# Kernel optimization log

Measured on AMD Instinct MI355X. Metric: run time of the kernel, lower is better.

## Reference

```python
import jax, jax.numpy as jnp
import numpy as np

L_OUTPUT = 1024  # SequenceDecoder l_output


def setup_inputs() -> dict:
    key = jax.random.key(0)
    k1, k2, k3 = jax.random.split(key, 3)
    B, L, D, DO = 16, 4096, 1024, 1024
    x = jax.random.normal(k1, (B, L, D), dtype=jnp.float32)
    # 0/1 padding-style mask; valid_length = mask.sum(axis=1)
    attention_mask = jax.random.randint(k2, (B, L), 0, 2, dtype=jnp.int32)
    # nn.Linear(d_model, d_output): weight (DO, D), bias (DO,)
    W = jax.random.normal(k3, (DO, D), dtype=jnp.float32) * (1.0 / np.sqrt(D))
    b = jnp.zeros((DO,), dtype=jnp.float32)
    return {"x": x, "attention_mask": attention_mask, "W": W, "b": b}


def _restrict_last(x, attention_mask, l_output):
    """Vectorized equivalent of the per-sample Python loop in mode='last':
    for each batch row i, take the LAST s_i = min(valid_len_i, l_output)
    elements of the full sequence, zero-padded at the tail to l_output.
    (When all s_i == l_output this matches x[:, -l_output:, :], which is the
    only case the original torch.stack-based loop handles without error.)"""
    B, L, D = x.shape
    valid = attention_mask.sum(axis=1)                    # (B,)
    s = jnp.minimum(valid, l_output)                      # (B,)
    j = jnp.arange(l_output)                              # (l_output,)
    idx = jnp.clip(L - s[:, None] + j[None, :], 0, L - 1) # (B, l_output)
    gathered = jnp.take_along_axis(x, idx[:, :, None], axis=1)  # (B, l_output, D)
    keep = (j[None, :] < s[:, None])[:, :, None]          # (B, l_output, 1)
    return jnp.where(keep, gathered, jnp.zeros((), dtype=x.dtype))


def reference(x, attention_mask, W, b):
    # mode='last' restrict, then output_transform = nn.Linear(d_model, d_output)
    restricted = _restrict_last(x, attention_mask, L_OUTPUT)  # (B, l_output, D)
    return jnp.einsum('bld,od->blo', restricted, W) + b       # (B, l_output, DO)
```

## Files before the change

### kernel.cpp

```cpp
#include <hip/hip_runtime.h>
#include <hip/hip_bf16.h>

#define L_SEQ   4096
#define D_IN    1024
#define N_BATCH 16
#define L_OUT   1024
#define D_OUT   1024
#define M_DIM   (N_BATCH * L_OUT)
#define K_DIM   D_IN

#define BM 256
#define BN 256
#define BK 64
#define NKT (K_DIM / BK)

typedef __attribute__((ext_vector_type(4))) float  f32x4;
typedef __attribute__((ext_vector_type(8))) __bf16 bf16x8;
typedef __attribute__((ext_vector_type(4))) __bf16 bf16x4;

#define WS_A_OFF 0u
#define WS_W_OFF (32u * 1024u * 1024u)
#define WS_S_OFF (WS_W_OFF + 2u * 1024u * 1024u)

__global__ __launch_bounds__(256) void mask_sum_kernel(
    const int* __restrict__ mask, int* __restrict__ s_out)
{
    const int b = blockIdx.x;
    const int t = threadIdx.x;
    const int* row = mask + (size_t)b * L_SEQ;

    int sum = 0;
#pragma unroll
    for (int i = 0; i < L_SEQ / 256; ++i) sum += row[t + i * 256];

#pragma unroll
    for (int off = 32; off > 0; off >>= 1) sum += __shfl_down(sum, off, 64);

    __shared__ int wsum[4];
    if ((t & 63) == 0) wsum[t >> 6] = sum;
    __syncthreads();
    if (t == 0) {
        int total = wsum[0] + wsum[1] + wsum[2] + wsum[3];
        s_out[b] = total < L_OUT ? total : L_OUT;
    }
}

__global__ __launch_bounds__(256) void convert_kernel(
    const float* __restrict__ x,
    const float* __restrict__ W,
    const int*   __restrict__ s_arr,
    __bf16* __restrict__ wsA,
    __bf16* __restrict__ wsW)
{
    const int rid = blockIdx.x;
    const int t   = threadIdx.x;
    const int e0  = t * 4;

    if (rid < M_DIM) {
        const int b = rid >> 10;
        const int j = rid & (L_OUT - 1);
        const int s = s_arr[b];
        const int rsw  = (rid & 7) << 3;
        const int dste = (e0 & ~63) | ((e0 & 63) ^ rsw);
        __bf16* dst = wsA + (size_t)rid * K_DIM + dste;
        if (j < s) {
            const float* src = x + ((size_t)b * L_SEQ + (L_SEQ - s + j)) * D_IN + e0;
            f32x4 v = *(const f32x4*)src;
            bf16x4 o = {(__bf16)v.x, (__bf16)v.y, (__bf16)v.z, (__bf16)v.w};
            *(bf16x4*)dst = o;
        } else {
            bf16x4 o = {(__bf16)0.f, (__bf16)0.f, (__bf16)0.f, (__bf16)0.f};
            *(bf16x4*)dst = o;
        }
    } else {
        const int n = rid - M_DIM;
        const int rsw  = (n & 7) << 3;
        const int dste = (e0 & ~63) | ((e0 & 63) ^ rsw);
        const float* src = W + (size_t)n * D_IN + e0;
        f32x4 v = *(const f32x4*)src;
        bf16x4 o = {(__bf16)v.x, (__bf16)v.y, (__bf16)v.z, (__bf16)v.w};
        *(bf16x4*)(wsW + (size_t)n * K_DIM + dste) = o;
    }
}

__device__ __forceinline__ void gload16(const __bf16* g, __bf16* l) {
    __builtin_amdgcn_global_load_lds(
        (const __attribute__((address_space(1))) void*)g,
        (__attribute__((address_space(3))) void*)l,
        16, 0, 0);
}

#define FENCE() asm volatile("" ::: "memory")

__global__ __launch_bounds__(512, 2) void gemm_kernel(
    const __bf16* __restrict__ A,
    const __bf16* __restrict__ Wb,
    const float*  __restrict__ bias,
    float* __restrict__ out)
{
    __shared__ __bf16 smem[2][2][BM * BK];

    const int t  = threadIdx.x;
    const int bx = blockIdx.x;
    const int vb = (bx & 7) * 32 + (bx >> 3);
    const int tile_n = vb & 3;
    const int tile_m = vb >> 2;
    const int m0 = tile_m * BM;
    const int n0 = tile_n * BN;
    const int lane = t & 63;
    const int wave = t >> 6;
    const int wm = wave >> 2;
    const int wn = wave & 3;

    const int srow = t >> 3;
    const int scol = (t & 7) * 8;
    const int sdst = (t & 7) * 8;

    const __bf16* Ag = A  + (size_t)m0 * K_DIM;
    const __bf16* Bg = Wb + (size_t)n0 * K_DIM;

#define STAGE_HALF(gbase, lbase, h, kt_)                                   \
    {                                                                      \
        _Pragma("unroll")                                                  \
        for (int rd = 0; rd < 2; ++rd) {                                   \
            const int r_ = (h) * 128 + rd * 64 + srow;                     \
            gload16((gbase) + (size_t)r_ * K_DIM + (kt_) * BK + scol,      \
                    (lbase) + r_ * BK + sdst);                             \
        }                                                                  \
    }

    const int fr  = lane & 15;
    const int k8  = (lane >> 4) * 8;
    const int swz = (fr & 7) << 3;
    const int kc0 = k8 ^ swz;
    const int kc1 = (32 + k8) ^ swz;

    float bias_v[4];
#pragma unroll
    for (int g = 0; g < 4; ++g)
        bias_v[g] = bias[n0 + wn * 64 + g * 16 + fr];

    bf16x8 aF[4][2], bF0[2][2], bF1[2][2];
    f32x4 acc[8][4];
#pragma unroll
    for (int f = 0; f < 8; ++f)
#pragma unroll
        for (int g = 0; g < 4; ++g) acc[f][g] = (f32x4){0.f, 0.f, 0.f, 0.f};

#define LOAD_AF(Ac, mh)                                                    \
    {                                                                      \
        const __bf16* rb_ = (Ac) + (wm * 128 + (mh) * 64 + fr) * BK;       \
        _Pragma("unroll")                                                  \
        for (int i = 0; i < 4; ++i) {                                      \
            aF[i][0] = *(const bf16x8*)&rb_[i * 16 * BK + kc0];            \
            aF[i][1] = *(const bf16x8*)&rb_[i * 16 * BK + kc1];            \
        }                                                                  \
    }

#define LOAD_BF(Bc, nh, bF)                                                \
    {                                                                      \
        const __bf16* rb_ = (Bc) + (wn * 64 + (nh) * 32 + fr) * BK;        \
        _Pragma("unroll")                                                  \
        for (int j = 0; j < 2; ++j) {                                      \
            bF[j][0] = *(const bf16x8*)&rb_[j * 16 * BK + kc0];            \
            bF[j][1] = *(const bf16x8*)&rb_[j * 16 * BK + kc1];            \
        }                                                                  \
    }

#define MFMA_QUAD(mh, nh, bF)                                              \
    {                                                                      \
        _Pragma("unroll")                                                  \
        for (int i = 0; i < 4; ++i)                                        \
            _Pragma("unroll")                                              \
            for (int j = 0; j < 2; ++j) {                                  \
                f32x4 c_ = acc[(mh) * 4 + i][(nh) * 2 + j];                \
                c_ = __builtin_amdgcn_mfma_f32_16x16x32_bf16(              \
                    aF[i][0], bF[j][0], c_, 0, 0, 0);                      \
                c_ = __builtin_amdgcn_mfma_f32_16x16x32_bf16(              \
                    aF[i][1], bF[j][1], c_, 0, 0, 0);                      \
                acc[(mh) * 4 + i][(nh) * 2 + j] = c_;                      \
            }                                                              \
    }

    {
        __bf16* A0l = &smem[0][0][0];
        __bf16* B0l = &smem[0][1][0];
        __bf16* A1l = &smem[1][0][0];
        __bf16* B1l = &smem[1][1][0];
        STAGE_HALF(Ag, A0l, 0, 0);
        STAGE_HALF(Bg, B0l, 1, 0);
        STAGE_HALF(Ag, A0l, 1, 0);
        STAGE_HALF(Bg, B0l, 0, 0);
        STAGE_HALF(Ag, A1l, 0, 1);
        STAGE_HALF(Bg, B1l, 1, 1);
    }

    for (int kt = 0; kt < NKT; ++kt) {
        const int cur = kt & 1;
        __bf16* Ac = &smem[cur][0][0];
        __bf16* Bc = &smem[cur][1][0];
        __bf16* An = &smem[cur ^ 1][0][0];
        __bf16* Bn = &smem[cur ^ 1][1][0];

        FENCE();
        if (kt == NKT - 1) asm volatile("s_waitcnt vmcnt(0)" ::: "memory");
        else               asm volatile("s_waitcnt vmcnt(4)" ::: "memory");
        __builtin_amdgcn_s_barrier();
        FENCE();
        LOAD_AF(Ac, 0);
        LOAD_BF(Bc, 0, bF0);
        if (kt + 1 < NKT) {
            STAGE_HALF(Ag, An, 1, kt + 1);
            STAGE_HALF(Bg, Bn, 0, kt + 1);
        }
        asm volatile("s_waitcnt lgkmcnt(0)" ::: "memory");
        __builtin_amdgcn_sched_barrier(0);
        __builtin_amdgcn_s_setprio(1);
        MFMA_QUAD(0, 0, bF0);
        __builtin_amdgcn_s_setprio(0);

        FENCE();
        __builtin_amdgcn_s_barrier();
        FENCE();
        LOAD_BF(Bc, 1, bF1);
        asm volatile("s_waitcnt lgkmcnt(0)" ::: "memory");
        __builtin_amdgcn_sched_barrier(0);
        __builtin_amdgcn_s_setprio(1);
        MFMA_QUAD(0, 1, bF1);
        __builtin_amdgcn_s_setprio(0);

        FENCE();
        __builtin_amdgcn_s_barrier();
        FENCE();
        LOAD_AF(Ac, 1);
        if (kt + 2 < NKT) STAGE_HALF(Ag, Ac, 0, kt + 2);
        asm volatile("s_waitcnt lgkmcnt(0)" ::: "memory");
        __builtin_amdgcn_sched_barrier(0);
        __builtin_amdgcn_s_setprio(1);
        MFMA_QUAD(1, 1, bF1);
        __builtin_amdgcn_s_setprio(0);

        FENCE();
        __builtin_amdgcn_s_barrier();
        FENCE();
        if (kt + 2 < NKT) STAGE_HALF(Bg, Bc, 1, kt + 2);
        __builtin_amdgcn_s_setprio(1);
        MFMA_QUAD(1, 0, bF0);
        __builtin_amdgcn_s_setprio(0);
    }

    const int row0 = m0 + wm * 128 + (lane >> 4) * 4;
    const int col0 = n0 + wn * 64 + fr;
#pragma unroll
    for (int f = 0; f < 8; ++f)
#pragma unroll
        for (int g = 0; g < 4; ++g)
#pragma unroll
            for (int rr = 0; rr < 4; ++rr)
                out[(size_t)(row0 + f * 16 + rr) * D_OUT + (col0 + g * 16)] =
                    acc[f][g][rr] + bias_v[g];

#undef STAGE_HALF
#undef LOAD_AF
#undef LOAD_BF
#undef MFMA_QUAD
}

extern "C" void kernel_launch(void* const* d_in, const int* in_sizes, int n_in,
                              void* d_out, int out_size, void* d_ws, size_t ws_size,
                              hipStream_t stream) {
    const float* x    = (const float*)d_in[0];
    const int*   mask = (const int*)d_in[1];
    const float* W    = (const float*)d_in[2];
    const float* bias = (const float*)d_in[3];
    float*       out  = (float*)d_out;

    __bf16* wsA   = (__bf16*)((char*)d_ws + WS_A_OFF);
    __bf16* wsW   = (__bf16*)((char*)d_ws + WS_W_OFF);
    int*    s_arr = (int*)((char*)d_ws + WS_S_OFF);

    mask_sum_kernel<<<dim3(N_BATCH), dim3(256), 0, stream>>>(mask, s_arr);

    convert_kernel<<<dim3(M_DIM + D_OUT), dim3(256), 0, stream>>>(
        x, W, s_arr, wsA, wsW);

    const int grid = (M_DIM / BM) * (D_OUT / BN);
    gemm_kernel<<<dim3(grid), dim3(512), 0, stream>>>(wsA, wsW, bias, out);
}
```

Measured before the change: 62.05 us.

## Fuse mask-sum, bf16 convert and GEMM into one cooperative kernel

Replaces the three launches (mask sum, fp32-to-bf16 convert with gather, GEMM) with a single cooperative kernel of 256 blocks that runs the phases separated by grid-wide syncs. The convert phase is redistributed so each GEMM block converts a slice of A and four rows of W with wider vectors. This removes launch gaps and inter-kernel tail effects, but adds two grid barriers and requires that all 256 blocks are co-resident (2 per CU).

```diff
diff --git a/kernel.cpp b/kernel.cpp
--- a/kernel.cpp
+++ b/kernel.cpp
@@ -1,5 +1,8 @@
 #include <hip/hip_runtime.h>
 #include <hip/hip_bf16.h>
+#include <hip/hip_cooperative_groups.h>
+
+namespace cg = cooperative_groups;
 
 #define L_SEQ   4096
 #define D_IN    1024
@@ -22,67 +25,6 @@
 #define WS_W_OFF (32u * 1024u * 1024u)
 #define WS_S_OFF (WS_W_OFF + 2u * 1024u * 1024u)
 
-__global__ __launch_bounds__(256) void mask_sum_kernel(
-    const int* __restrict__ mask, int* __restrict__ s_out)
-{
-    const int b = blockIdx.x;
-    const int t = threadIdx.x;
-    const int* row = mask + (size_t)b * L_SEQ;
-
-    int sum = 0;
-#pragma unroll
-    for (int i = 0; i < L_SEQ / 256; ++i) sum += row[t + i * 256];
-
-#pragma unroll
-    for (int off = 32; off > 0; off >>= 1) sum += __shfl_down(sum, off, 64);
-
-    __shared__ int wsum[4];
-    if ((t & 63) == 0) wsum[t >> 6] = sum;
-    __syncthreads();
-    if (t == 0) {
-        int total = wsum[0] + wsum[1] + wsum[2] + wsum[3];
-        s_out[b] = total < L_OUT ? total : L_OUT;
-    }
-}
-
-__global__ __launch_bounds__(256) void convert_kernel(
-    const float* __restrict__ x,
-    const float* __restrict__ W,
-    const int*   __restrict__ s_arr,
-    __bf16* __restrict__ wsA,
-    __bf16* __restrict__ wsW)
-{
-    const int rid = blockIdx.x;
-    const int t   = threadIdx.x;
-    const int e0  = t * 4;
-
-    if (rid < M_DIM) {
-        const int b = rid >> 10;
-        const int j = rid & (L_OUT - 1);
-        const int s = s_arr[b];
-        const int rsw  = (rid & 7) << 3;
-        const int dste = (e0 & ~63) | ((e0 & 63) ^ rsw);
-        __bf16* dst = wsA + (size_t)rid * K_DIM + dste;
-        if (j < s) {
-            const float* src = x + ((size_t)b * L_SEQ + (L_SEQ - s + j)) * D_IN + e0;
-            f32x4 v = *(const f32x4*)src;
-            bf16x4 o = {(__bf16)v.x, (__bf16)v.y, (__bf16)v.z, (__bf16)v.w};
-            *(bf16x4*)dst = o;
-        } else {
-            bf16x4 o = {(__bf16)0.f, (__bf16)0.f, (__bf16)0.f, (__bf16)0.f};
-            *(bf16x4*)dst = o;
-        }
-    } else {
-        const int n = rid - M_DIM;
-        const int rsw  = (n & 7) << 3;
-        const int dste = (e0 & ~63) | ((e0 & 63) ^ rsw);
-        const float* src = W + (size_t)n * D_IN + e0;
-        f32x4 v = *(const f32x4*)src;
-        bf16x4 o = {(__bf16)v.x, (__bf16)v.y, (__bf16)v.z, (__bf16)v.w};
-        *(bf16x4*)(wsW + (size_t)n * K_DIM + dste) = o;
-    }
-}
-
 __device__ __forceinline__ void gload16(const __bf16* g, __bf16* l) {
     __builtin_amdgcn_global_load_lds(
         (const __attribute__((address_space(1))) void*)g,
@@ -92,17 +34,82 @@
 
 #define FENCE() asm volatile("" ::: "memory")
 
-__global__ __launch_bounds__(512, 2) void gemm_kernel(
-    const __bf16* __restrict__ A,
-    const __bf16* __restrict__ Wb,
-    const float*  __restrict__ bias,
-    float* __restrict__ out)
+__global__ __launch_bounds__(512, 2) void fused_kernel(
+    const float* __restrict__ x,
+    const int*   __restrict__ mask,
+    const float* __restrict__ W,
+    const float* __restrict__ bias,
+    int*         __restrict__ s_arr,
+    __bf16*      __restrict__ wsA,
+    __bf16*      __restrict__ wsW,
+    float*       __restrict__ out)
 {
     __shared__ __bf16 smem[2][2][BM * BK];
+
+    cg::grid_group grid = cg::this_grid();
 
     const int t  = threadIdx.x;
     const int bx = blockIdx.x;
     const int vb = (bx & 7) * 32 + (bx >> 3);
+
+    if (bx < N_BATCH) {
+        const int4* row = (const int4*)(mask + (size_t)bx * L_SEQ);
+        int4 v0 = row[t];
+        int4 v1 = row[t + 512];
+        int sum = v0.x + v0.y + v0.z + v0.w + v1.x + v1.y + v1.z + v1.w;
+#pragma unroll
+        for (int off = 32; off > 0; off >>= 1) sum += __shfl_down(sum, off, 64);
+        int* wsum = (int*)&smem[0][0][0];
+        if ((t & 63) == 0) wsum[t >> 6] = sum;
+        __syncthreads();
+        if (t == 0) {
+            int total = 0;
+#pragma unroll
+            for (int w = 0; w < 8; ++w) total += wsum[w];
+            s_arr[bx] = total < L_OUT ? total : L_OUT;
+        }
+    }
+    __threadfence();
+    grid.sync();
+
+    {
+        const int wrow = vb * 4 + (t >> 7);
+        const int we0  = (t & 127) * 8;
+        const int wrsw = (wrow & 7) << 3;
+        const int wdst = (we0 & ~63) | ((we0 & 63) ^ wrsw);
+        f32x4 wv0 = *(const f32x4*)(W + (size_t)wrow * D_IN + we0);
+        f32x4 wv1 = *(const f32x4*)(W + (size_t)wrow * D_IN + we0 + 4);
+        bf16x8 wo = {(__bf16)wv0.x, (__bf16)wv0.y, (__bf16)wv0.z, (__bf16)wv0.w,
+                     (__bf16)wv1.x, (__bf16)wv1.y, (__bf16)wv1.z, (__bf16)wv1.w};
+        *(bf16x8*)(wsW + (size_t)wrow * K_DIM + wdst) = wo;
+
+        const int pm = vb >> 2;
+        const int kq = vb & 3;
+        const int am0 = pm * 256;
+        const int b  = am0 >> 10;
+        const int s  = s_arr[b];
+        const float* xb = x + ((size_t)b * L_SEQ + (size_t)(L_SEQ - s)) * D_IN;
+        const int e0 = kq * 256 + (t & 63) * 4;
+        const bf16x4 zo = {(__bf16)0.f, (__bf16)0.f, (__bf16)0.f, (__bf16)0.f};
+#pragma unroll 4
+        for (int sweep = 0; sweep < 32; ++sweep) {
+            const int rl = (t >> 6) + sweep * 8;
+            const int m  = am0 + rl;
+            const int j  = m & (L_OUT - 1);
+            const int dste = (e0 & ~63) | ((e0 & 63) ^ ((m & 7) << 3));
+            __bf16* dst = wsA + (size_t)m * K_DIM + dste;
+            if (j < s) {
+                f32x4 v = *(const f32x4*)(xb + (size_t)j * D_IN + e0);
+                bf16x4 o = {(__bf16)v.x, (__bf16)v.y, (__bf16)v.z, (__bf16)v.w};
+                *(bf16x4*)dst = o;
+            } else {
+                *(bf16x4*)dst = zo;
+            }
+        }
+    }
+    __threadfence();
+    grid.sync();
+
     const int tile_n = vb & 3;
     const int tile_m = vb >> 2;
     const int m0 = tile_m * BM;
@@ -114,10 +121,9 @@
 
     const int srow = t >> 3;
     const int scol = (t & 7) * 8;
-    const int sdst = (t & 7) * 8;
-
-    const __bf16* Ag = A  + (size_t)m0 * K_DIM;
-    const __bf16* Bg = Wb + (size_t)n0 * K_DIM;
+
+    const __bf16* Ag = wsA + (size_t)m0 * K_DIM;
+    const __bf16* Bg = wsW + (size_t)n0 * K_DIM;
 
 #define STAGE_HALF(gbase, lbase, h, kt_)                                   \
     {                                                                      \
@@ -125,7 +131,7 @@
         for (int rd = 0; rd < 2; ++rd) {                                   \
             const int r_ = (h) * 128 + rd * 64 + srow;                     \
             gload16((gbase) + (size_t)r_ * K_DIM + (kt_) * BK + scol,      \
-                    (lbase) + r_ * BK + sdst);                             \
+                    (lbase) + r_ * BK + scol);                             \
         }                                                                  \
     }
 
@@ -279,11 +285,8 @@
     __bf16* wsW   = (__bf16*)((char*)d_ws + WS_W_OFF);
     int*    s_arr = (int*)((char*)d_ws + WS_S_OFF);
 
-    mask_sum_kernel<<<dim3(N_BATCH), dim3(256), 0, stream>>>(mask, s_arr);
-
-    convert_kernel<<<dim3(M_DIM + D_OUT), dim3(256), 0, stream>>>(
-        x, W, s_arr, wsA, wsW);
-
-    const int grid = (M_DIM / BM) * (D_OUT / BN);
-    gemm_kernel<<<dim3(grid), dim3(512), 0, stream>>>(wsA, wsW, bias, out);
+    void* args[] = {(void*)&x, (void*)&mask, (void*)&W, (void*)&bias,
+                    (void*)&s_arr, (void*)&wsA, (void*)&wsW, (void*)&out};
+    hipLaunchCooperativeKernel((const void*)fused_kernel,
+                               dim3(256), dim3(512), args, 0, stream);
 }
```

New measurement: 219.3 us. 253% more time.
